# Kernel optimization log

Hardware: AMD Instinct MI355X
Metric: run time of the kernel (lower is better)

Reference implementation:

```python
import jax, jax.numpy as jnp
import numpy as np

N = 100000      # num nodes
E = 600000      # num edges
DIN = 64        # input_dim
DH = 128        # hidden_dim
G = 512         # num graphs
EPS = 1e-5      # BatchNorm eps


def setup_inputs() -> dict:
    key = jax.random.key(0)
    ks = jax.random.split(key, 12)
    x = jax.random.normal(ks[0], (N, DIN), jnp.float32)
    edge_index = jax.random.randint(ks[1], (2, E), 0, N)
    batch = jnp.sort(jax.random.randint(ks[2], (N,), 0, G))

    def w(k, shape):
        return (jax.random.normal(k, shape, jnp.float32) / np.float32(np.sqrt(shape[0])))

    inp = {"x": x, "edge_index": edge_index, "batch": batch}
    inp.update(
        W1=w(ks[3], (DIN, DH)), b1=jnp.zeros((DH,), jnp.float32),
        bn1_g=jnp.ones((DH,), jnp.float32), bn1_b=jnp.zeros((DH,), jnp.float32),
        bn1_m=jax.random.normal(ks[4], (DH,), jnp.float32) * 0.1,
        bn1_v=jnp.ones((DH,), jnp.float32),
        W2=w(ks[5], (DH, DH)), b2=jnp.zeros((DH,), jnp.float32),
        bn2_g=jnp.ones((DH,), jnp.float32), bn2_b=jnp.zeros((DH,), jnp.float32),
        bn2_m=jax.random.normal(ks[6], (DH,), jnp.float32) * 0.1,
        bn2_v=jnp.ones((DH,), jnp.float32),
        W3=w(ks[7], (DH, DH)), b3=jnp.zeros((DH,), jnp.float32),
        bn3_g=jnp.ones((DH,), jnp.float32), bn3_b=jnp.zeros((DH,), jnp.float32),
        bn3_m=jax.random.normal(ks[8], (DH,), jnp.float32) * 0.1,
        bn3_v=jnp.ones((DH,), jnp.float32),
        fc1_w=w(ks[9], (DH, DH // 2)), fc1_b=jnp.zeros((DH // 2,), jnp.float32),
        fc2_w=w(ks[10], (DH // 2, 1)), fc2_b=jnp.zeros((1,), jnp.float32),
    )
    return inp


def reference(x, edge_index, batch,
              W1, b1, bn1_g, bn1_b, bn1_m, bn1_v,
              W2, b2, bn2_g, bn2_b, bn2_m, bn2_v,
              W3, b3, bn3_g, bn3_b, bn3_m, bn3_v,
              fc1_w, fc1_b, fc2_w, fc2_b):
    # --- GCN normalization with self-loops (PyG GCNConv, sym norm) ---
    loop = jnp.arange(N, dtype=edge_index.dtype)
    src = jnp.concatenate([edge_index[0], loop])  # [E+N]
    dst = jnp.concatenate([edge_index[1], loop])  # [E+N]
    deg = jax.ops.segment_sum(jnp.ones_like(dst, jnp.float32), dst, num_segments=N)
    dis = jnp.where(deg > 0, jax.lax.rsqrt(jnp.maximum(deg, 1.0)), 0.0)
    norm = (dis[src] * dis[dst])[:, None]  # [E+N, 1]

    def conv(h, W, b):
        h = h @ W
        agg = jax.ops.segment_sum(h[src] * norm, dst, num_segments=N)
        return agg + b

    def bn(h, g, bta, m, v):
        return (h - m) * jax.lax.rsqrt(v + EPS) * g + bta  # eval-mode BatchNorm1d

    # block 1 (dropout is identity in eval)
    h = jax.nn.relu(bn(conv(x, W1, b1), bn1_g, bn1_b, bn1_m, bn1_v))
    # middle residual block (num_layers=3 -> one block)
    h = jax.nn.relu(bn(conv(h, W2, b2), bn2_g, bn2_b, bn2_m, bn2_v)) + h
    # output conv block
    h = jax.nn.relu(bn(conv(h, W3, b3), bn3_g, bn3_b, bn3_m, bn3_v))

    # global mean pool over graphs
    sums = jax.ops.segment_sum(h, batch, num_segments=G)          # [G, DH]
    cnt = jax.ops.segment_sum(jnp.ones((N, 1), h.dtype), batch, num_segments=G)
    pooled = sums / jnp.maximum(cnt, 1.0)

    h = jax.nn.relu(pooled @ fc1_w + fc1_b)
    return jax.nn.sigmoid(h @ fc2_w + fc2_b)  # [G, 1]
```

## Files before the change

### kernel.cpp

```cpp
#include <hip/hip_runtime.h>
#include <math.h>

#define N_NODES 100000
#define N_EDGES 600000
#define DIN     64
#define DH      128
#define NG      512
#define EPS_BN  1e-5f
#define SCAN_TPB 256
#define N_SCAN_BLK ((N_NODES + SCAN_TPB - 1) / SCAN_TPB)
#define G_EDGE   ((N_EDGES + 255) / 256)

typedef unsigned short u16;
typedef short s16x8 __attribute__((ext_vector_type(8)));
typedef float f32x4 __attribute__((ext_vector_type(4)));
typedef int   i32x4 __attribute__((ext_vector_type(4)));
typedef signed char s8x8 __attribute__((ext_vector_type(8)));

__device__ __forceinline__ u16 f2bf(float x) {
    unsigned u = __builtin_bit_cast(unsigned, x);
    u += 0x7fffu + ((u >> 16) & 1u);
    return (u16)(u >> 16);
}
__device__ __forceinline__ float bf2f(u16 h) {
    unsigned u = ((unsigned)h) << 16;
    return __builtin_bit_cast(float, u);
}

#define ZERO_INTS (2 * N_NODES + 256)
__global__ __launch_bounds__(256) void zero_kernel(int* __restrict__ p) {
    const int i = (blockIdx.x * 256 + threadIdx.x) * 4;
    if (i < ZERO_INTS) *(i32x4*)(p + i) = i32x4{0, 0, 0, 0};
}

#define PREP_WT1_BLKS  32
#define PREP_WT2_BLKS  64
#define PREP_WT3_BLKS  64
#define PREP_BN_BLKS   2
#define PREP_GB_BLKS   3
#define PREP_B0 G_EDGE
#define PREP_B1 (PREP_B0 + PREP_WT1_BLKS)
#define PREP_B2 (PREP_B1 + PREP_WT2_BLKS)
#define PREP_B3 (PREP_B2 + PREP_WT3_BLKS)
#define PREP_B4 (PREP_B3 + PREP_BN_BLKS)
#define PREP_TOTAL (PREP_B4 + PREP_GB_BLKS)

__device__ __forceinline__ void wt_body(const float* __restrict__ W, u16* __restrict__ Wt,
                                        int K, int idx) {
    if (idx >= K * DH) return;
    int k = idx / DH, n = idx % DH;
    Wt[(long)n * K + k] = f2bf(W[idx]);
}

__global__ __launch_bounds__(256) void degprep_kernel(
    const int* __restrict__ dst, int* __restrict__ deg,
    const float* __restrict__ W1, u16* __restrict__ Wt1,
    const float* __restrict__ W2, u16* __restrict__ Wt2,
    const float* __restrict__ W3, u16* __restrict__ Wt3,
    const float* b1, const float* g1, const float* bb1, const float* m1, const float* v1,
    const float* b2, const float* g2, const float* bb2, const float* m2, const float* v2,
    const float* b3, const float* g3, const float* bb3, const float* m3, const float* v3,
    float* __restrict__ sc, float* __restrict__ sh,
    const int* __restrict__ batch, int* __restrict__ gp) {
    const int b = blockIdx.x;
    const int tid = threadIdx.x;
    if (b < PREP_B0) {
        const int e = b * 256 + tid;
        if (e < N_EDGES) atomicAdd(&deg[dst[e]], 1);
    } else if (b < PREP_B1) {
        wt_body(W1, Wt1, DIN, (b - PREP_B0) * 256 + tid);
    } else if (b < PREP_B2) {
        wt_body(W2, Wt2, DH, (b - PREP_B1) * 256 + tid);
    } else if (b < PREP_B3) {
        wt_body(W3, Wt3, DH, (b - PREP_B2) * 256 + tid);
    } else if (b < PREP_B4) {
        const int i = (b - PREP_B3) * 256 + tid;
        if (i < 3 * DH) {
            int l = i >> 7, c = i & (DH - 1);
            const float* bc = l == 0 ? b1 : (l == 1 ? b2 : b3);
            const float* g  = l == 0 ? g1 : (l == 1 ? g2 : g3);
            const float* bb = l == 0 ? bb1 : (l == 1 ? bb2 : bb3);
            const float* m  = l == 0 ? m1 : (l == 1 ? m2 : m3);
            const float* v  = l == 0 ? v1 : (l == 1 ? v2 : v3);
            float s = g[c] * rsqrtf(v[c] + EPS_BN);
            sc[i] = s;
            sh[i] = (bc[c] - m[c]) * s + bb[c];
        }
    } else {
        const int g = (b - PREP_B4) * 256 + tid;
        if (g <= NG) {
            int lo = 0, hi = N_NODES;
            while (lo < hi) {
                int mid = (lo + hi) >> 1;
                if (batch[mid] < g) lo = mid + 1; else hi = mid;
            }
            gp[g] = lo;
        }
    }
}

__global__ __launch_bounds__(SCAN_TPB) void scan_kernel(const int* __restrict__ deg,
                                                        float* __restrict__ dis,
                                                        int* __restrict__ rp,
                                                        int* __restrict__ blk,
                                                        int* __restrict__ done, int n) {
    __shared__ int sm[SCAN_TPB];
    __shared__ int sflag;
    const int t = threadIdx.x;
    const int i = blockIdx.x * SCAN_TPB + t;
    int v = 0;
    if (i < n) {
        v = deg[i];
        dis[i] = rsqrtf((float)v + 1.0f);
    }
    sm[t] = v;
    __syncthreads();
#pragma unroll
    for (int off = 1; off < SCAN_TPB; off <<= 1) {
        int u = (t >= off) ? sm[t - off] : 0;
        __syncthreads();
        sm[t] += u;
        __syncthreads();
    }
    if (i <= n) rp[i] = sm[t] - v;
    if (t == SCAN_TPB - 1) blk[blockIdx.x] = sm[t];

    __syncthreads();
    if (t == 0) {
        __threadfence();
        const int r = atomicAdd(done, 1);
        sflag = (r == (int)gridDim.x - 1);
    }
    __syncthreads();
    if (!sflag) return;

    int a0 = (2 * t < N_SCAN_BLK)
                 ? __hip_atomic_load(&blk[2 * t], __ATOMIC_RELAXED, __HIP_MEMORY_SCOPE_AGENT)
                 : 0;
    int a1 = (2 * t + 1 < N_SCAN_BLK)
                 ? __hip_atomic_load(&blk[2 * t + 1], __ATOMIC_RELAXED, __HIP_MEMORY_SCOPE_AGENT)
                 : 0;
    const int s = a0 + a1;
    sm[t] = s;
    __syncthreads();
#pragma unroll
    for (int off = 1; off < SCAN_TPB; off <<= 1) {
        int u = (t >= off) ? sm[t - off] : 0;
        __syncthreads();
        sm[t] += u;
        __syncthreads();
    }
    const int ex = sm[t] - s;
    if (2 * t < N_SCAN_BLK) blk[2 * t] = ex;
    if (2 * t + 1 < N_SCAN_BLK) blk[2 * t + 1] = ex + a0;
}

#define CSRX_XCVT_BLKS 3125
#define CSRX_TOTAL (G_EDGE + CSRX_XCVT_BLKS)
__global__ __launch_bounds__(256) void csr_xcvt_kernel(const int* __restrict__ src,
                                                       const int* __restrict__ dst,
                                                       const int* __restrict__ rp,
                                                       const int* __restrict__ blk,
                                                       int* __restrict__ cursor,
                                                       int* __restrict__ col,
                                                       const float* __restrict__ x,
                                                       const float* __restrict__ dis,
                                                       u16* __restrict__ xb) {
    const int b = blockIdx.x;
    const int tid = threadIdx.x;
    if (b < G_EDGE) {
        const int e = b * 256 + tid;
        if (e >= N_EDGES) return;
        const int s = src[e];
        const int d = dst[e];
        const int p = atomicAdd(&cursor[d], 1);
        col[rp[d] + blk[d >> 8] + p] = s;
    } else {
        const long base = ((long)(b - G_EDGE) * 256 + tid) * 8;
        const float dd = dis[base >> 6];
        const float4 a = *(const float4*)(x + base);
        const float4 c = *(const float4*)(x + base + 4);
        s16x8 o;
        o[0] = (short)f2bf(a.x * dd); o[1] = (short)f2bf(a.y * dd);
        o[2] = (short)f2bf(a.z * dd); o[3] = (short)f2bf(a.w * dd);
        o[4] = (short)f2bf(c.x * dd); o[5] = (short)f2bf(c.y * dd);
        o[6] = (short)f2bf(c.z * dd); o[7] = (short)f2bf(c.w * dd);
        *(s16x8*)(xb + base) = o;
    }
}

__global__ __launch_bounds__(256) void agg64_kernel(const u16* __restrict__ xb,
                                                    const int* __restrict__ rp,
                                                    const int* __restrict__ blk,
                                                    const int* __restrict__ col,
                                                    const float* __restrict__ dis,
                                                    u16* __restrict__ aggX, int n) {
    const long t = (long)blockIdx.x * blockDim.x + threadIdx.x;
    const int lane = (int)(t & 31);
    const long i = t >> 5;
    if (i >= n) return;
    const int cl = lane & 7;
    const int eh = (lane >> 3) & 3;
    const int c = cl * 8;

    float acc[8] = {0, 0, 0, 0, 0, 0, 0, 0};
    if (eh == 0) {
        const s16x8 hv = *(const s16x8*)(xb + i * DIN + c);
#pragma unroll
        for (int q = 0; q < 8; ++q) acc[q] = bf2f((u16)hv[q]);
    }

    const int beg = rp[i] + blk[i >> 8];
    const int end = rp[i + 1] + blk[(int)(i + 1) >> 8];
    for (int e = beg + eh; e < end; e += 4) {
        const int s = col[e];
        const s16x8 v = *(const s16x8*)(xb + (long)s * DIN + c);
#pragma unroll
        for (int q = 0; q < 8; ++q) acc[q] += bf2f((u16)v[q]);
    }

#pragma unroll
    for (int q = 0; q < 8; ++q) acc[q] += __shfl_xor(acc[q], 8);
#pragma unroll
    for (int q = 0; q < 8; ++q) acc[q] += __shfl_xor(acc[q], 16);

    if (eh == 0 && (lane >> 4) == 0) {
        const float dd = dis[i];
        s16x8 ov;
#pragma unroll
        for (int q = 0; q < 8; ++q) ov[q] = (short)f2bf(acc[q] * dd);
        *(s16x8*)(aggX + i * DIN + c) = ov;
    }
}

template <int K, bool BN_EPI, bool QOUT>
__global__ __launch_bounds__(256) void gemm_mfma(const u16* __restrict__ A,
                                                 const u16* __restrict__ Wt,
                                                 const float* __restrict__ dis,
                                                 const float* __restrict__ scl,
                                                 const float* __restrict__ shf,
                                                 u16* __restrict__ C,
                                                 signed char* __restrict__ Cq,
                                                 float* __restrict__ qsc,
                                                 int M) {
    __shared__ u16 ldsc[4][16][DH];
    const int wave = threadIdx.x >> 6;
    const int lane = threadIdx.x & 63;
    const int r16 = lane & 15;
    const int kc  = lane >> 4;
    const long row0 = (long)blockIdx.x * 64 + wave * 16;

    f32x4 acc[8];
#pragma unroll
    for (int t = 0; t < 8; ++t)
#pragma unroll
        for (int q = 0; q < 4; ++q) acc[t][q] = 0.0f;

    long arow = row0 + r16;
    if (arow >= M) arow = M - 1;

#pragma unroll
    for (int ks = 0; ks < K; ks += 32) {
        const s16x8 a = *(const s16x8*)(A + arow * K + ks + kc * 8);
#pragma unroll
        for (int t = 0; t < 8; ++t) {
            const s16x8 b = *(const s16x8*)(Wt + (long)(t * 16 + r16) * K + ks + kc * 8);
            acc[t] = __builtin_amdgcn_mfma_f32_16x16x32_bf16(a, b, acc[t], 0, 0, 0);
        }
    }

    float dd[4], scv[8], shv[8];
    if constexpr (BN_EPI) {
#pragma unroll
        for (int t = 0; t < 8; ++t) {
            scv[t] = scl[t * 16 + r16];
            shv[t] = shf[t * 16 + r16];
        }
    } else {
#pragma unroll
        for (int q = 0; q < 4; ++q) {
            long r = row0 + kc * 4 + q;
            dd[q] = dis[r < M ? r : (M - 1)];
        }
    }

#pragma unroll
    for (int t = 0; t < 8; ++t) {
        const int blkc = (t << 1) | (r16 >> 3);
        const int co = r16 & 7;
#pragma unroll
        for (int q = 0; q < 4; ++q) {
            const int row = kc * 4 + q;
            float y;
            if constexpr (BN_EPI) {
                y = fmaxf(fmaf(acc[t][q], scv[t], shv[t]), 0.0f);
            } else {
                y = acc[t][q] * dd[q];
            }
            ldsc[wave][row][(((blkc ^ (row & 7)) << 3) | co)] = f2bf(y);
        }
    }
#pragma unroll
    for (int it = 0; it < 4; ++it) {
        const int rl = (lane >> 4) + it * 4;
        const long row = row0 + rl;
        const int phys = (lane & 15) ^ (rl & 7);
        const s16x8 v = *(const s16x8*)&ldsc[wave][rl][phys << 3];
        if constexpr (QOUT) {
            float f[8], m = 0.0f;
#pragma unroll
            for (int q = 0; q < 8; ++q) {
                f[q] = bf2f((u16)v[q]);
                m = fmaxf(m, fabsf(f[q]));
            }
            m = fmaxf(m, __shfl_xor(m, 1));
            m = fmaxf(m, __shfl_xor(m, 2));
            m = fmaxf(m, __shfl_xor(m, 4));
            m = fmaxf(m, __shfl_xor(m, 8));
            const float inv = (m > 0.0f) ? 127.0f / m : 0.0f;
            s8x8 o;
#pragma unroll
            for (int q = 0; q < 8; ++q) o[q] = (signed char)(int)rintf(f[q] * inv);
            if (row < M) {
                *(s8x8*)(Cq + row * DH + ((lane & 15) << 3)) = o;
                if ((lane & 15) == 0) qsc[row] = m * (1.0f / 127.0f);
            }
        } else {
            if (row < M) *(s16x8*)(C + row * DH + ((lane & 15) << 3)) = v;
        }
    }
}

template <bool RES>
__global__ __launch_bounds__(256) void agg_epi_q8_kernel(const signed char* __restrict__ Hq,
                                                         const float* __restrict__ qsc,
                                                         const int* __restrict__ rp,
                                                         const int* __restrict__ blk,
                                                         const int* __restrict__ col,
                                                         const float* __restrict__ dis,
                                                         const float* __restrict__ scl,
                                                         const float* __restrict__ shf,
                                                         u16* __restrict__ out, int n) {
    const long t = (long)blockIdx.x * blockDim.x + threadIdx.x;
    const int lane = (int)(t & 31);
    const long i = t >> 5;
    if (i >= n) return;
    const int cl = lane & 15;
    const int eh = lane >> 4;
    const int c = cl * 8;

    float acc[8] = {0, 0, 0, 0, 0, 0, 0, 0};
    if (eh == 0) {
        const s8x8 hv = *(const s8x8*)(Hq + i * DH + c);
        const float hs = qsc[i];
#pragma unroll
        for (int q = 0; q < 8; ++q) acc[q] = (float)hv[q] * hs;
    }

    const int beg = rp[i] + blk[i >> 8];
    const int end = rp[i + 1] + blk[(int)(i + 1) >> 8];
    for (int e = beg + eh; e < end; e += 2) {
        const int s = col[e];
        const float ss = qsc[s];
        const s8x8 v = *(const s8x8*)(Hq + (long)s * DH + c);
#pragma unroll
        for (int q = 0; q < 8; ++q) acc[q] = fmaf((float)v[q], ss, acc[q]);
    }

#pragma unroll
    for (int q = 0; q < 8; ++q) acc[q] += __shfl_xor(acc[q], 16);

    if (eh == 0) {
        const float dd = dis[i];
        const float4 s0 = *(const float4*)(scl + c);
        const float4 s1 = *(const float4*)(scl + c + 4);
        const float4 f0 = *(const float4*)(shf + c);
        const float4 f1 = *(const float4*)(shf + c + 4);
        const float sv[8] = {s0.x, s0.y, s0.z, s0.w, s1.x, s1.y, s1.z, s1.w};
        const float fv[8] = {f0.x, f0.y, f0.z, f0.w, f1.x, f1.y, f1.z, f1.w};

        float r[8];
#pragma unroll
        for (int q = 0; q < 8; ++q) r[q] = fmaxf(fmaf(acc[q] * dd, sv[q], fv[q]), 0.0f);
        if (RES) {
            const s16x8 rv = *(const s16x8*)(out + i * DH + c);
#pragma unroll
            for (int q = 0; q < 8; ++q) r[q] += bf2f((u16)rv[q]);
        }
        s16x8 ov;
#pragma unroll
        for (int q = 0; q < 8; ++q) ov[q] = (short)f2bf(r[q]);
        __builtin_nontemporal_store(ov, (s16x8*)(out + i * DH + c));
    }
}

__global__ __launch_bounds__(256) void pool_head_kernel(const u16* __restrict__ h,
                                                        const int* __restrict__ gp,
                                                        const float* __restrict__ fc1w,
                                                        const float* __restrict__ fc1b,
                                                        const float* __restrict__ fc2w,
                                                        const float* __restrict__ fc2b,
                                                        float* __restrict__ out) {
    const int g = blockIdx.x;
    const int t = threadIdx.x;
    const int grp = t >> 4;
    const int cl = t & 15;
    const int c = cl * 8;
    const int beg = gp[g];
    const int end = gp[g + 1];

    float acc[8] = {0, 0, 0, 0, 0, 0, 0, 0};
    for (int i = beg + grp; i < end; i += 16) {
        const s16x8 v = *(const s16x8*)(h + (long)i * DH + c);
#pragma unroll
        for (int q = 0; q < 8; ++q) acc[q] += bf2f((u16)v[q]);
    }

    __shared__ float sm[16][DH];
    __shared__ float p[DH];
#pragma unroll
    for (int q = 0; q < 8; ++q) sm[grp][c + q] = acc[q];
    __syncthreads();

    if (t < DH) {
        float s = 0.0f;
#pragma unroll
        for (int r = 0; r < 16; ++r) s += sm[r][t];
        p[t] = s / fmaxf((float)(end - beg), 1.0f);
    }
    __syncthreads();

    if (t < 64) {
        float a = 0.0f;
#pragma unroll 4
        for (int k = 0; k < DH; ++k) a = fmaf(p[k], fc1w[(long)k * 64 + t], a);
        const float h1 = fmaxf(a + fc1b[t], 0.0f);
        float v = h1 * fc2w[t];
#pragma unroll
        for (int off = 32; off > 0; off >>= 1) v += __shfl_down(v, off);
        if (t == 0) out[g] = 1.0f / (1.0f + expf(-(v + fc2b[0])));
    }
}

extern "C" void kernel_launch(void* const* d_in, const int* in_sizes, int n_in,
                              void* d_out, int out_size, void* d_ws, size_t ws_size,
                              hipStream_t stream) {
    const float* x     = (const float*)d_in[0];
    const int*   ei    = (const int*)d_in[1];
    const int*   batch = (const int*)d_in[2];
    const float* W1 = (const float*)d_in[3];
    const float* b1 = (const float*)d_in[4];
    const float* g1 = (const float*)d_in[5];
    const float* t1 = (const float*)d_in[6];
    const float* m1 = (const float*)d_in[7];
    const float* v1 = (const float*)d_in[8];
    const float* W2 = (const float*)d_in[9];
    const float* b2 = (const float*)d_in[10];
    const float* g2 = (const float*)d_in[11];
    const float* t2 = (const float*)d_in[12];
    const float* m2 = (const float*)d_in[13];
    const float* v2 = (const float*)d_in[14];
    const float* W3 = (const float*)d_in[15];
    const float* b3 = (const float*)d_in[16];
    const float* g3 = (const float*)d_in[17];
    const float* t3 = (const float*)d_in[18];
    const float* m3 = (const float*)d_in[19];
    const float* v3 = (const float*)d_in[20];
    const float* fc1w = (const float*)d_in[21];
    const float* fc1b = (const float*)d_in[22];
    const float* fc2w = (const float*)d_in[23];
    const float* fc2b = (const float*)d_in[24];

    const int* src = ei;
    const int* dst = ei + N_EDGES;

    char* ws = (char*)d_ws;
    size_t off = 0;
    auto alloc = [&](size_t bytes) -> char* {
        char* p = ws + off;
        off = (off + bytes + 511) & ~(size_t)511;
        return p;
    };
    int*   deg     = (int*)  alloc((size_t)ZERO_INTS * 4);
    int*   cursor  = deg + N_NODES;
    int*   done    = deg + 2 * N_NODES;
    float* dis     = (float*)alloc((size_t)N_NODES * 4);
    int*   rp      = (int*)  alloc(((size_t)N_NODES + 1) * 4);
    int*   blk     = (int*)  alloc((size_t)N_SCAN_BLK * 4);
    int*   col     = (int*)  alloc((size_t)N_EDGES * 4);
    int*   gp      = (int*)  alloc((size_t)(NG + 1) * 4);
    float* bnsc    = (float*)alloc((size_t)3 * DH * 4);
    float* bnsh    = (float*)alloc((size_t)3 * DH * 4);
    u16*   Wt1     = (u16*)  alloc((size_t)DH * DIN * 2);
    u16*   Wt2     = (u16*)  alloc((size_t)DH * DH * 2);
    u16*   Wt3     = (u16*)  alloc((size_t)DH * DH * 2);
    u16*   xb      = (u16*)  alloc((size_t)N_NODES * DIN * 2);
    u16*   aggX    = (u16*)  alloc((size_t)N_NODES * DIN * 2);
    signed char* bufQ = (signed char*)alloc((size_t)N_NODES * DH);
    float* qscale  = (float*)alloc((size_t)N_NODES * 4);
    u16*   bufA    = (u16*)  alloc((size_t)N_NODES * DH * 2);

    const int TPB = 256;
    const int gZero = (ZERO_INTS / 4 + TPB - 1) / TPB;
    const int gGemm = (N_NODES + 63) / 64;
    const int gAgg  = (int)(((long)N_NODES * 32 + TPB - 1) / TPB);

    zero_kernel<<<gZero, TPB, 0, stream>>>(deg);
    degprep_kernel<<<PREP_TOTAL, TPB, 0, stream>>>(dst, deg, W1, Wt1, W2, Wt2, W3, Wt3,
                                                   b1, g1, t1, m1, v1,
                                                   b2, g2, t2, m2, v2,
                                                   b3, g3, t3, m3, v3,
                                                   bnsc, bnsh, batch, gp);
    scan_kernel<<<N_SCAN_BLK, SCAN_TPB, 0, stream>>>(deg, dis, rp, blk, done, N_NODES);
    csr_xcvt_kernel<<<CSRX_TOTAL, TPB, 0, stream>>>(src, dst, rp, blk, cursor, col,
                                                    x, dis, xb);

    agg64_kernel<<<gAgg, TPB, 0, stream>>>(xb, rp, blk, col, dis, aggX, N_NODES);
    gemm_mfma<DIN, true, false><<<gGemm, TPB, 0, stream>>>(aggX, Wt1, dis, bnsc, bnsh,
                                                           bufA, nullptr, nullptr, N_NODES);
    gemm_mfma<DH, false, true><<<gGemm, TPB, 0, stream>>>(bufA, Wt2, dis, nullptr, nullptr,
                                                          nullptr, bufQ, qscale, N_NODES);
    agg_epi_q8_kernel<true><<<gAgg, TPB, 0, stream>>>(bufQ, qscale, rp, blk, col, dis,
                                                      bnsc + DH, bnsh + DH, bufA, N_NODES);
    gemm_mfma<DH, false, true><<<gGemm, TPB, 0, stream>>>(bufA, Wt3, dis, nullptr, nullptr,
                                                          nullptr, bufQ, qscale, N_NODES);
    agg_epi_q8_kernel<false><<<gAgg, TPB, 0, stream>>>(bufQ, qscale, rp, blk, col, dis,
                                                       bnsc + 2 * DH, bnsh + 2 * DH, bufA,
                                                       N_NODES);

    pool_head_kernel<<<NG, TPB, 0, stream>>>(bufA, gp, fc1w, fc1b, fc2w, fc2b,
                                             (float*)d_out);
}
```

Before: 285.4 us.

## Process two 16-row tiles per wave in MFMA GEMM to reuse weight loads

The GEMM kernel now has each wave compute 32 rows (two 16-row MFMA tiles) instead of 16, so each loaded weight fragment feeds two MFMAs. This halves the grid size and the weight-load traffic per output row. The cost is doubled accumulator registers, which may lower occupancy. Separately, the CSR column scatter write becomes a nontemporal store to reduce cache pollution.

Result: slower. 294.4 us (+3.2%).

```diff
diff --git a/kernel.cpp b/kernel.cpp
--- a/kernel.cpp
+++ b/kernel.cpp
@@ -174,7 +174,7 @@
         const int s = src[e];
         const int d = dst[e];
         const int p = atomicAdd(&cursor[d], 1);
-        col[rp[d] + blk[d >> 8] + p] = s;
+        __builtin_nontemporal_store(s, &col[rp[d] + blk[d >> 8] + p]);
     } else {
         const long base = ((long)(b - G_EDGE) * 256 + tid) * 8;
         const float dd = dis[base >> 6];
@@ -248,85 +248,95 @@
     const int lane = threadIdx.x & 63;
     const int r16 = lane & 15;
     const int kc  = lane >> 4;
-    const long row0 = (long)blockIdx.x * 64 + wave * 16;
-
-    f32x4 acc[8];
-#pragma unroll
-    for (int t = 0; t < 8; ++t)
-#pragma unroll
-        for (int q = 0; q < 4; ++q) acc[t][q] = 0.0f;
-
-    long arow = row0 + r16;
-    if (arow >= M) arow = M - 1;
+    const long row0 = (long)blockIdx.x * 128 + wave * 32;
+
+    f32x4 acc[2][8];
+#pragma unroll
+    for (int h = 0; h < 2; ++h)
+#pragma unroll
+        for (int t = 0; t < 8; ++t)
+#pragma unroll
+            for (int q = 0; q < 4; ++q) acc[h][t][q] = 0.0f;
+
+    long arow0 = row0 + r16;      if (arow0 >= M) arow0 = M - 1;
+    long arow1 = row0 + 16 + r16; if (arow1 >= M) arow1 = M - 1;
 
 #pragma unroll
     for (int ks = 0; ks < K; ks += 32) {
-        const s16x8 a = *(const s16x8*)(A + arow * K + ks + kc * 8);
+        const s16x8 a0 = *(const s16x8*)(A + arow0 * K + ks + kc * 8);
+        const s16x8 a1 = *(const s16x8*)(A + arow1 * K + ks + kc * 8);
 #pragma unroll
         for (int t = 0; t < 8; ++t) {
             const s16x8 b = *(const s16x8*)(Wt + (long)(t * 16 + r16) * K + ks + kc * 8);
-            acc[t] = __builtin_amdgcn_mfma_f32_16x16x32_bf16(a, b, acc[t], 0, 0, 0);
-        }
-    }
-
-    float dd[4], scv[8], shv[8];
+            acc[0][t] = __builtin_amdgcn_mfma_f32_16x16x32_bf16(a0, b, acc[0][t], 0, 0, 0);
+            acc[1][t] = __builtin_amdgcn_mfma_f32_16x16x32_bf16(a1, b, acc[1][t], 0, 0, 0);
+        }
+    }
+
+    float scv[8], shv[8];
     if constexpr (BN_EPI) {
 #pragma unroll
         for (int t = 0; t < 8; ++t) {
             scv[t] = scl[t * 16 + r16];
             shv[t] = shf[t * 16 + r16];
         }
-    } else {
-#pragma unroll
-        for (int q = 0; q < 4; ++q) {
-            long r = row0 + kc * 4 + q;
-            dd[q] = dis[r < M ? r : (M - 1)];
-        }
-    }
-
-#pragma unroll
-    for (int t = 0; t < 8; ++t) {
-        const int blkc = (t << 1) | (r16 >> 3);
-        const int co = r16 & 7;
-#pragma unroll
-        for (int q = 0; q < 4; ++q) {
-            const int row = kc * 4 + q;
-            float y;
-            if constexpr (BN_EPI) {
-                y = fmaxf(fmaf(acc[t][q], scv[t], shv[t]), 0.0f);
+    }
+
+#pragma unroll
+    for (int h = 0; h < 2; ++h) {
+        const long rbase = row0 + h * 16;
+        float dd[4];
+        if constexpr (!BN_EPI) {
+#pragma unroll
+            for (int q = 0; q < 4; ++q) {
+                long r = rbase + kc * 4 + q;
+                dd[q] = dis[r < M ? r : (M - 1)];
+            }
+        }
+#pragma unroll
+        for (int t = 0; t < 8; ++t) {
+            const int blkc = (t << 1) | (r16 >> 3);
+            const int co = r16 & 7;
+#pragma unroll
+            for (int q = 0; q < 4; ++q) {
+                const int row = kc * 4 + q;
+                float y;
+                if constexpr (BN_EPI) {
+                    y = fmaxf(fmaf(acc[h][t][q], scv[t], shv[t]), 0.0f);
+                } else {
+                    y = acc[h][t][q] * dd[q];
+                }
+                ldsc[wave][row][(((blkc ^ (row & 7)) << 3) | co)] = f2bf(y);
+            }
+        }
+#pragma unroll
+        for (int it = 0; it < 4; ++it) {
+            const int rl = (lane >> 4) + it * 4;
+            const long row = rbase + rl;
+            const int phys = (lane & 15) ^ (rl & 7);
+            const s16x8 v = *(const s16x8*)&ldsc[wave][rl][phys << 3];
+            if constexpr (QOUT) {
+                float f[8], m = 0.0f;
+#pragma unroll
+                for (int q = 0; q < 8; ++q) {
+                    f[q] = bf2f((u16)v[q]);
+                    m = fmaxf(m, fabsf(f[q]));
+                }
+                m = fmaxf(m, __shfl_xor(m, 1));
+                m = fmaxf(m, __shfl_xor(m, 2));
+                m = fmaxf(m, __shfl_xor(m, 4));
+                m = fmaxf(m, __shfl_xor(m, 8));
+                const float inv = (m > 0.0f) ? 127.0f / m : 0.0f;
+                s8x8 o;
+#pragma unroll
+                for (int q = 0; q < 8; ++q) o[q] = (signed char)(int)rintf(f[q] * inv);
+                if (row < M) {
+                    *(s8x8*)(Cq + row * DH + ((lane & 15) << 3)) = o;
+                    if ((lane & 15) == 0) qsc[row] = m * (1.0f / 127.0f);
+                }
             } else {
-                y = acc[t][q] * dd[q];
+                if (row < M) *(s16x8*)(C + row * DH + ((lane & 15) << 3)) = v;
             }
-            ldsc[wave][row][(((blkc ^ (row & 7)) << 3) | co)] = f2bf(y);
-        }
-    }
-#pragma unroll
-    for (int it = 0; it < 4; ++it) {
-        const int rl = (lane >> 4) + it * 4;
-        const long row = row0 + rl;
-        const int phys = (lane & 15) ^ (rl & 7);
-        const s16x8 v = *(const s16x8*)&ldsc[wave][rl][phys << 3];
-        if constexpr (QOUT) {
-            float f[8], m = 0.0f;
-#pragma unroll
-            for (int q = 0; q < 8; ++q) {
-                f[q] = bf2f((u16)v[q]);
-                m = fmaxf(m, fabsf(f[q]));
-            }
-            m = fmaxf(m, __shfl_xor(m, 1));
-            m = fmaxf(m, __shfl_xor(m, 2));
-            m = fmaxf(m, __shfl_xor(m, 4));
-            m = fmaxf(m, __shfl_xor(m, 8));
-            const float inv = (m > 0.0f) ? 127.0f / m : 0.0f;
-            s8x8 o;
-#pragma unroll
-            for (int q = 0; q < 8; ++q) o[q] = (signed char)(int)rintf(f[q] * inv);
-            if (row < M) {
-                *(s8x8*)(Cq + row * DH + ((lane & 15) << 3)) = o;
-                if ((lane & 15) == 0) qsc[row] = m * (1.0f / 127.0f);
-            }
-        } else {
-            if (row < M) *(s16x8*)(C + row * DH + ((lane & 15) << 3)) = v;
         }
     }
 }
@@ -502,7 +512,7 @@
 
     const int TPB = 256;
     const int gZero = (ZERO_INTS / 4 + TPB - 1) / TPB;
-    const int gGemm = (N_NODES + 63) / 64;
+    const int gGemm = (N_NODES + 127) / 128;
     const int gAgg  = (int)(((long)N_NODES * 32 + TPB - 1) / TPB);
 
     zero_kernel<<<gZero, TPB, 0, stream>>>(deg);
```
